# Kernel optimization log

Hardware: AMD Instinct MI355X
Metric: run time of the kernel (lower is better)

The kernel has to match this reference:

```python
import jax, jax.numpy as jnp
import numpy as np

EMBED_DIM = 1024
NUM_HEADS = 16
HEAD_DIM = EMBED_DIM // NUM_HEADS
B, S = 2, 2048


def setup_inputs() -> dict:
    key = jax.random.key(0)
    ks = jax.random.split(key, 9)
    d = EMBED_DIM
    scale = 1.0 / np.sqrt(d)
    inp = {
        "x": jax.random.normal(ks[0], (B, S, d), dtype=jnp.float32),
        "mask": jnp.ones((B, S), dtype=jnp.int32),
        "Wq": jax.random.normal(ks[1], (d, d), dtype=jnp.float32) * scale,
        "bq": jnp.zeros((d,), dtype=jnp.float32),
        "Wk": jax.random.normal(ks[2], (d, d), dtype=jnp.float32) * scale,
        "bk": jnp.zeros((d,), dtype=jnp.float32),
        "Wv": jax.random.normal(ks[3], (d, d), dtype=jnp.float32) * scale,
        "bv": jnp.zeros((d,), dtype=jnp.float32),
        "Wo": jax.random.normal(ks[4], (d, d), dtype=jnp.float32) * scale,
        "bo": jnp.zeros((d,), dtype=jnp.float32),
    }
    return inp


def reference(x, mask, Wq, bq, Wk, bk, Wv, bv, Wo, bo):
    b, s, _ = x.shape
    # projections; torch Linear computes x @ W.T + b
    q = (x @ Wq.T + bq).reshape(b, s, NUM_HEADS, HEAD_DIM).transpose(0, 2, 1, 3)
    k = (x @ Wk.T + bk).reshape(b, s, NUM_HEADS, HEAD_DIM).transpose(0, 2, 1, 3)
    v = (x @ Wv.T + bv).reshape(b, s, NUM_HEADS, HEAD_DIM).transpose(0, 2, 1, 3)
    scores = jnp.einsum("bhqd,bhkd->bhqk", q, k) / np.sqrt(HEAD_DIM)  # (B,H,S,S)
    m = (mask == 0)[:, None, None, :]  # broadcast over heads and query pos
    scores = jnp.where(m, jnp.float32(-1e9), scores)
    attn = jax.nn.softmax(scores, axis=-1)
    out = jnp.einsum("bhqk,bhkd->bhqd", attn, v)
    out = out.transpose(0, 2, 1, 3).reshape(b, s, EMBED_DIM)
    return out @ Wo.T + bo
```

## Files before the change

### kernel.cpp

```cpp
#include <hip/hip_runtime.h>

#define EMBED 1024
#define NHEAD 16
#define HDIM  64
#define BB    2
#define SS    2048

typedef __bf16 bf16x8 __attribute__((ext_vector_type(8)));
typedef float  f32x4  __attribute__((ext_vector_type(4)));
typedef _Float16 f16x4 __attribute__((ext_vector_type(4)));
typedef __fp16 hf16x2 __attribute__((ext_vector_type(2)));

#if defined(__has_builtin)
#if __has_builtin(__builtin_amdgcn_exp2f)
#define EXP2(x) __builtin_amdgcn_exp2f(x)
#else
#define EXP2(x) exp2f(x)
#endif
#else
#define EXP2(x) exp2f(x)
#endif

__device__ __forceinline__ unsigned short f2bf(float f) {
  union { float f; unsigned u; } v; v.f = f;
  unsigned r = v.u + 0x7fffu + ((v.u >> 16) & 1u);
  return (unsigned short)(r >> 16);
}

__device__ __forceinline__ unsigned short f2h(float f) {
  union { _Float16 h; unsigned short u; } t;
  t.h = (_Float16)f;
  return t.u;
}

__device__ __forceinline__ void g2l16(const unsigned short* g, unsigned short* l) {
  __builtin_amdgcn_global_load_lds(
      (const __attribute__((address_space(1))) unsigned int*)g,
      (__attribute__((address_space(3))) unsigned int*)l, 16, 0, 0);
}

__global__ __launch_bounds__(256)
void cvt5_kernel(const float* __restrict__ x,  const float* __restrict__ Wq,
                 const float* __restrict__ Wk, const float* __restrict__ Wv,
                 const float* __restrict__ Wo, const int* __restrict__ mask,
                 unsigned short* __restrict__ xb,  unsigned short* __restrict__ Wqb,
                 unsigned short* __restrict__ Wkb, unsigned short* __restrict__ Wvb,
                 unsigned short* __restrict__ Wob, float* __restrict__ mbias) {
  const int i = blockIdx.x * 256 + threadIdx.x;
  if (i < (1 << 21)) {
    const float* src;
    unsigned short* dst;
    int j;
    if (i < (1 << 20)) {
      src = x; dst = xb; j = i;
    } else {
      const int t = i - (1 << 20);
      const int r = t >> 18;
      j = t & ((1 << 18) - 1);
      src = (r == 0) ? Wq : (r == 1) ? Wk : (r == 2) ? Wv : Wo;
      dst = (r == 0) ? Wqb : (r == 1) ? Wkb : (r == 2) ? Wvb : Wob;
    }
    const float4 f = ((const float4*)src)[j];
    ushort4 u;
    u.x = f2bf(f.x); u.y = f2bf(f.y); u.z = f2bf(f.z); u.w = f2bf(f.w);
    ((ushort4*)dst)[j] = u;
  } else {
    const int j = i - (1 << 21);
    const int4 m = ((const int4*)mask)[j];
    float4 o;
    o.x = m.x ? 0.f : -1e30f; o.y = m.y ? 0.f : -1e30f;
    o.z = m.z ? 0.f : -1e30f; o.w = m.w ? 0.f : -1e30f;
    ((float4*)mbias)[j] = o;
  }
}

template <typename EpiFn>
__device__ __forceinline__
void gemm_core(const unsigned short* __restrict__ A,
               const unsigned short* __restrict__ Bm,
               int m0, int n0, EpiFn epi) {
  __shared__ unsigned short sA[128 * 64];
  __shared__ unsigned short sB[128 * 64];
  const int tid = threadIdx.x;
  const int l  = tid & 63;
  const int w  = tid >> 6;
  const int lm = l & 15;
  const int qd = l >> 4;
  const int wm = w & 1;
  const int wn = w >> 1;

  f32x4 acc[4][4];
#pragma unroll
  for (int i = 0; i < 4; ++i)
#pragma unroll
    for (int j = 0; j < 4; ++j) acc[i][j] = (f32x4){0.f, 0.f, 0.f, 0.f};

  for (int k0 = 0; k0 < EMBED; k0 += 64) {
#pragma unroll
    for (int i = 0; i < 4; ++i) {
      const int t = i * 256 + tid;
      const int r = t >> 3;
      const int c = (t & 7) ^ (r & 7);
      g2l16(A + (m0 + r) * EMBED + k0 + c * 8, &sA[(i * 256 + (w << 6)) * 8]);
      g2l16(Bm + (n0 + r) * EMBED + k0 + c * 8, &sB[(i * 256 + (w << 6)) * 8]);
    }
    __syncthreads();
#pragma unroll
    for (int kk = 0; kk < 2; ++kk) {
      bf16x8 af[4], bfr[4];
#pragma unroll
      for (int mi = 0; mi < 4; ++mi) {
        const int R = wm * 64 + mi * 16 + lm;
        const int ch = R * 8 + (((kk << 2) + qd) ^ (R & 7));
        af[mi] = *(const bf16x8*)&sA[ch * 8];
      }
#pragma unroll
      for (int ni = 0; ni < 4; ++ni) {
        const int R = wn * 64 + ni * 16 + lm;
        const int ch = R * 8 + (((kk << 2) + qd) ^ (R & 7));
        bfr[ni] = *(const bf16x8*)&sB[ch * 8];
      }
#pragma unroll
      for (int mi = 0; mi < 4; ++mi)
#pragma unroll
        for (int ni = 0; ni < 4; ++ni)
          acc[mi][ni] = __builtin_amdgcn_mfma_f32_16x16x32_bf16(
              af[mi], bfr[ni], acc[mi][ni], 0, 0, 0);
    }
    __syncthreads();
  }

#pragma unroll
  for (int mi = 0; mi < 4; ++mi)
#pragma unroll
    for (int ni = 0; ni < 4; ++ni) {
      const int mb = m0 + wm * 64 + mi * 16 + qd * 4;
      const int n  = n0 + wn * 64 + ni * 16 + lm;
      epi(acc[mi][ni], mb, n);
    }
}

__device__ __forceinline__ void decode_tile(int flat, int& a0, int& b0) {
  const int sub = flat & 15;
  const int g = flat >> 4;
  a0 = ((g >> 2) * 2 + (sub >> 3));
  b0 = ((g & 3) * 8 + (sub & 7));
}

__global__ __launch_bounds__(256)
void gemm_qkv(const unsigned short* __restrict__ xb,
              const unsigned short* __restrict__ Wqb,
              const unsigned short* __restrict__ Wkb,
              const unsigned short* __restrict__ Wvb,
              const float* __restrict__ bq, const float* __restrict__ bk,
              const float* __restrict__ bv,
              unsigned short* __restrict__ Qb, unsigned short* __restrict__ Kb,
              unsigned short* __restrict__ VTb) {
  const int z = blockIdx.y;
  int a0, b0;
  decode_tile(blockIdx.x, a0, b0);
  if (z < 2) {
    const unsigned short* A = z ? Wkb : Wqb;
    const float* bias = z ? bk : bq;
    unsigned short* O = z ? Kb : Qb;
    const float scale = z ? 1.0f : 0.125f * 1.4426950408889634f;
    gemm_core(A, xb, a0 * 128, b0 * 128, [&](const f32x4& v, int mb, int n) {
      const float4 bvv = *(const float4*)&bias[mb];
      const int h = mb >> 6, d0 = mb & 63;
      const int b = n >> 11, s = n & 2047;
      ushort4 u;
      u.x = f2bf((v.x + bvv.x) * scale); u.y = f2bf((v.y + bvv.y) * scale);
      u.z = f2bf((v.z + bvv.z) * scale); u.w = f2bf((v.w + bvv.w) * scale);
      *(ushort4*)&O[(((b * NHEAD + h) * SS) + s) * HDIM + d0] = u;
    });
  } else {
    gemm_core(xb, Wvb, b0 * 128, a0 * 128, [&](const f32x4& v, int mb, int n) {
      const float bvv = bv[n];
      const int b = mb >> 11, s = mb & 2047;
      const int h = n >> 6, d = n & 63;
      ushort4 u;
      u.x = f2h(v.x + bvv); u.y = f2h(v.y + bvv);
      u.z = f2h(v.z + bvv); u.w = f2h(v.w + bvv);
      *(ushort4*)&VTb[(((b * NHEAD + h) * HDIM) + d) * SS + s] = u;
    });
  }
}

__global__ __launch_bounds__(256)
void gemm_out(const unsigned short* __restrict__ Wob,
              const unsigned short* __restrict__ Ob,
              const float* __restrict__ bo, float* __restrict__ out) {
  int a0, b0;
  decode_tile(blockIdx.x, a0, b0);
  gemm_core(Wob, Ob, a0 * 128, b0 * 128, [&](const f32x4& v, int mb, int n) {
    const float4 bvv = *(const float4*)&bo[mb];
    float4 o;
    o.x = v.x + bvv.x; o.y = v.y + bvv.y; o.z = v.z + bvv.z; o.w = v.w + bvv.w;
    *(float4*)&out[n * EMBED + mb] = o;
  });
}

__global__ __launch_bounds__(256)
void attn_kernel(const unsigned short* __restrict__ Q,
                 const unsigned short* __restrict__ K,
                 const unsigned short* __restrict__ VT,
                 const float* __restrict__ mbias,
                 unsigned short* __restrict__ Obuf) {
  __shared__ unsigned short sK[64 * 64];
  __shared__ unsigned short sV[64 * 64];
  const int tid = threadIdx.x;
  const int l = tid & 63, w = tid >> 6;
  const int lm = l & 15, qd = l >> 4;
  const int b = blockIdx.z, h = blockIdx.y;
  const int q0 = blockIdx.x * 128 + w * 32;
  const unsigned short* Qh = Q + ((b * NHEAD + h) * SS) * HDIM;
  const unsigned short* Kh = K + ((b * NHEAD + h) * SS) * HDIM;
  const unsigned short* Vh = VT + ((b * NHEAD + h) * HDIM) * SS;
  const float* mb = mbias + b * SS;

  bf16x8 qf[2][2];
#pragma unroll
  for (int g = 0; g < 2; ++g) {
    qf[g][0] = *(const bf16x8*)&Qh[(q0 + g * 16 + lm) * HDIM + qd * 8];
    qf[g][1] = *(const bf16x8*)&Qh[(q0 + g * 16 + lm) * HDIM + 32 + qd * 8];
  }

  f32x4 Od[2][4];
#pragma unroll
  for (int g = 0; g < 2; ++g)
#pragma unroll
    for (int i = 0; i < 4; ++i) Od[g][i] = (f32x4){0.f, 0.f, 0.f, 0.f};
  float lsum[2] = {0.f, 0.f};

  for (int kb = 0; kb < SS; kb += 64) {
#pragma unroll
    for (int i = 0; i < 2; ++i) {
      const int t = i * 256 + tid;
      const int r = t >> 3;
      const int c = (t & 7) ^ (r & 7);
      g2l16(Kh + (kb + r) * HDIM + c * 8, &sK[(i * 256 + (w << 6)) * 8]);
      g2l16(Vh + r * SS + kb + c * 8, &sV[(i * 256 + (w << 6)) * 8]);
    }
    __syncthreads();

    f16x4 pf[2][4];
#pragma unroll
    for (int j = 0; j < 4; ++j) {
      const int R = j * 16 + lm;
      const bf16x8 k0 = *(const bf16x8*)&sK[(R * 8 + (qd ^ (lm & 7))) * 8];
      const bf16x8 k1 = *(const bf16x8*)&sK[(R * 8 + ((4 + qd) ^ (lm & 7))) * 8];
      const float4 bj = *(const float4*)&mb[kb + j * 16 + qd * 4];
      const f32x4 binit = (f32x4){bj.x, bj.y, bj.z, bj.w};
#pragma unroll
      for (int g = 0; g < 2; ++g) {
        f32x4 t0 = binit;
        t0 = __builtin_amdgcn_mfma_f32_16x16x32_bf16(k0, qf[g][0], t0, 0, 0, 0);
        t0 = __builtin_amdgcn_mfma_f32_16x16x32_bf16(k1, qf[g][1], t0, 0, 0, 0);
        const float p0 = EXP2(t0[0]);
        const float p1 = EXP2(t0[1]);
        const float p2 = EXP2(t0[2]);
        const float p3 = EXP2(t0[3]);
        lsum[g] += (p0 + p1) + (p2 + p3);
        union { hf16x2 v[2]; f16x4 f; } pk;
        pk.v[0] = __builtin_amdgcn_cvt_pkrtz(p0, p1);
        pk.v[1] = __builtin_amdgcn_cvt_pkrtz(p2, p3);
        pf[g][j] = pk.f;
      }
    }

#pragma unroll
    for (int dt = 0; dt < 4; ++dt) {
      const int row = dt * 16 + lm;
#pragma unroll
      for (int j = 0; j < 4; ++j) {
        const int ch = (j * 2 + (qd >> 1)) ^ (lm & 7);
        const f16x4 vf = *(const f16x4*)&sV[row * 64 + ch * 8 + (qd & 1) * 4];
#pragma unroll
        for (int g = 0; g < 2; ++g)
          Od[g][dt] = __builtin_amdgcn_mfma_f32_16x16x16f16(vf, pf[g][j],
                                                            Od[g][dt], 0, 0, 0);
      }
    }
    __syncthreads();
  }

#pragma unroll
  for (int g = 0; g < 2; ++g) {
    float ls = lsum[g];
    ls += __shfl_xor(ls, 16);
    ls += __shfl_xor(ls, 32);
    const float rinv = 1.f / ls;
#pragma unroll
    for (int dt = 0; dt < 4; ++dt) {
      ushort4 u;
      u.x = f2bf(Od[g][dt][0] * rinv); u.y = f2bf(Od[g][dt][1] * rinv);
      u.z = f2bf(Od[g][dt][2] * rinv); u.w = f2bf(Od[g][dt][3] * rinv);
      *(ushort4*)&Obuf[(b * SS + q0 + g * 16 + lm) * EMBED + h * HDIM +
                       dt * 16 + qd * 4] = u;
    }
  }
}

extern "C" void kernel_launch(void* const* d_in, const int* in_sizes, int n_in,
                              void* d_out, int out_size, void* d_ws, size_t ws_size,
                              hipStream_t stream) {
  const float* x  = (const float*)d_in[0];
  const int* mask = (const int*)d_in[1];
  const float* Wq = (const float*)d_in[2];
  const float* bq = (const float*)d_in[3];
  const float* Wk = (const float*)d_in[4];
  const float* bk = (const float*)d_in[5];
  const float* Wv = (const float*)d_in[6];
  const float* bv = (const float*)d_in[7];
  const float* Wo = (const float*)d_in[8];
  const float* bo = (const float*)d_in[9];
  float* out = (float*)d_out;

  char* ws = (char*)d_ws;
  unsigned short* xb  = (unsigned short*)(ws);
  unsigned short* Wqb = (unsigned short*)(ws + 8u * 1024 * 1024);
  unsigned short* Wkb = Wqb + 1024 * 1024;
  unsigned short* Wvb = Wkb + 1024 * 1024;
  unsigned short* Wob = Wvb + 1024 * 1024;
  unsigned short* Qb  = (unsigned short*)(ws + 16u * 1024 * 1024);
  unsigned short* Kb  = Qb + 4u * 1024 * 1024;
  unsigned short* VTb = Kb + 4u * 1024 * 1024;
  unsigned short* Ob  = VTb + 4u * 1024 * 1024;
  float* mbb = (float*)(ws + 48u * 1024 * 1024);

  cvt5_kernel<<<8196, 256, 0, stream>>>(x, Wq, Wk, Wv, Wo, mask,
                                        xb, Wqb, Wkb, Wvb, Wob, mbb);
  gemm_qkv<<<dim3(256, 3), 256, 0, stream>>>(xb, Wqb, Wkb, Wvb, bq, bk, bv,
                                             Qb, Kb, VTb);
  attn_kernel<<<dim3(16, 16, 2), 256, 0, stream>>>(Qb, Kb, VTb, mbb, Ob);
  gemm_out<<<256, 256, 0, stream>>>(Wob, Ob, bo, out);
}
```

Baseline: 219.8 us.

## Split attention along the key dimension into two partials and add combine kernel

The attention kernel now splits the key sequence into two halves across an extra grid dimension, doubling the number of blocks. Each half writes an unnormalized bf16 output and its row sums. A new combine kernel adds the two partials and normalizes them before the output projection. The aim is more blocks per CU and better latency hiding on the attention stage. The cost is an extra kernel launch, extra global traffic for the partial buffers, and bf16 rounding of the unnormalized partial outputs.

After: 218.5 us. No clear change (-0.6%).

```diff
diff --git a/kernel.cpp b/kernel.cpp
--- a/kernel.cpp
+++ b/kernel.cpp
@@ -25,6 +25,11 @@
   union { float f; unsigned u; } v; v.f = f;
   unsigned r = v.u + 0x7fffu + ((v.u >> 16) & 1u);
   return (unsigned short)(r >> 16);
+}
+
+__device__ __forceinline__ float bf2f(unsigned short u) {
+  union { unsigned u; float f; } v; v.u = ((unsigned)u) << 16;
+  return v.f;
 }
 
 __device__ __forceinline__ unsigned short f2h(float f) {
@@ -205,18 +210,21 @@
                  const unsigned short* __restrict__ K,
                  const unsigned short* __restrict__ VT,
                  const float* __restrict__ mbias,
-                 unsigned short* __restrict__ Obuf) {
+                 unsigned short* __restrict__ Opart,
+                 float* __restrict__ Lpart) {
   __shared__ unsigned short sK[64 * 64];
   __shared__ unsigned short sV[64 * 64];
   const int tid = threadIdx.x;
   const int l = tid & 63, w = tid >> 6;
   const int lm = l & 15, qd = l >> 4;
-  const int b = blockIdx.z, h = blockIdx.y;
+  const int b = blockIdx.z & 1, sp = blockIdx.z >> 1, h = blockIdx.y;
   const int q0 = blockIdx.x * 128 + w * 32;
   const unsigned short* Qh = Q + ((b * NHEAD + h) * SS) * HDIM;
   const unsigned short* Kh = K + ((b * NHEAD + h) * SS) * HDIM;
   const unsigned short* Vh = VT + ((b * NHEAD + h) * HDIM) * SS;
   const float* mb = mbias + b * SS;
+  unsigned short* Op = Opart + sp * (BB * SS * EMBED);
+  float* Lp = Lpart + sp * (BB * NHEAD * SS);
 
   bf16x8 qf[2][2];
 #pragma unroll
@@ -232,7 +240,8 @@
     for (int i = 0; i < 4; ++i) Od[g][i] = (f32x4){0.f, 0.f, 0.f, 0.f};
   float lsum[2] = {0.f, 0.f};
 
-  for (int kb = 0; kb < SS; kb += 64) {
+  const int kend = sp * (SS / 2) + (SS / 2);
+  for (int kb = sp * (SS / 2); kb < kend; kb += 64) {
 #pragma unroll
     for (int i = 0; i < 2; ++i) {
       const int t = i * 256 + tid;
@@ -289,16 +298,43 @@
     float ls = lsum[g];
     ls += __shfl_xor(ls, 16);
     ls += __shfl_xor(ls, 32);
-    const float rinv = 1.f / ls;
+    if (qd == 0) Lp[(b * NHEAD + h) * SS + q0 + g * 16 + lm] = ls;
 #pragma unroll
     for (int dt = 0; dt < 4; ++dt) {
       ushort4 u;
-      u.x = f2bf(Od[g][dt][0] * rinv); u.y = f2bf(Od[g][dt][1] * rinv);
-      u.z = f2bf(Od[g][dt][2] * rinv); u.w = f2bf(Od[g][dt][3] * rinv);
-      *(ushort4*)&Obuf[(b * SS + q0 + g * 16 + lm) * EMBED + h * HDIM +
-                       dt * 16 + qd * 4] = u;
-    }
-  }
+      u.x = f2bf(Od[g][dt][0]); u.y = f2bf(Od[g][dt][1]);
+      u.z = f2bf(Od[g][dt][2]); u.w = f2bf(Od[g][dt][3]);
+      *(ushort4*)&Op[(b * SS + q0 + g * 16 + lm) * EMBED + h * HDIM +
+                     dt * 16 + qd * 4] = u;
+    }
+  }
+}
+
+__global__ __launch_bounds__(256)
+void combine_kernel(const unsigned short* __restrict__ Opart,
+                    const float* __restrict__ Lpart,
+                    unsigned short* __restrict__ Ob) {
+  const int i = blockIdx.x * 256 + threadIdx.x;
+  const int base = i * 8;
+  const int token = base >> 10;
+  const int h = (base >> 6) & 15;
+  const int b = token >> 11, q = token & 2047;
+  const int lidx = (b * NHEAD + h) * SS + q;
+  const float ls = Lpart[lidx] + Lpart[BB * NHEAD * SS + lidx];
+  const float rinv = 1.f / ls;
+  const ushort4* p0 = (const ushort4*)&Opart[base];
+  const ushort4* p1 = (const ushort4*)&Opart[BB * SS * EMBED + base];
+  ushort4 o[2];
+#pragma unroll
+  for (int k = 0; k < 2; ++k) {
+    const ushort4 a = p0[k], c = p1[k];
+    o[k].x = f2bf((bf2f(a.x) + bf2f(c.x)) * rinv);
+    o[k].y = f2bf((bf2f(a.y) + bf2f(c.y)) * rinv);
+    o[k].z = f2bf((bf2f(a.z) + bf2f(c.z)) * rinv);
+    o[k].w = f2bf((bf2f(a.w) + bf2f(c.w)) * rinv);
+  }
+  *(ushort4*)&Ob[base] = o[0];
+  *(ushort4*)&Ob[base + 4] = o[1];
 }
 
 extern "C" void kernel_launch(void* const* d_in, const int* in_sizes, int n_in,
@@ -317,21 +353,26 @@
   float* out = (float*)d_out;
 
   char* ws = (char*)d_ws;
+  const size_t MB = 1024 * 1024;
   unsigned short* xb  = (unsigned short*)(ws);
-  unsigned short* Wqb = (unsigned short*)(ws + 8u * 1024 * 1024);
+  unsigned short* Ob  = (unsigned short*)(ws);
+  unsigned short* Wqb = (unsigned short*)(ws + 8 * MB);
   unsigned short* Wkb = Wqb + 1024 * 1024;
   unsigned short* Wvb = Wkb + 1024 * 1024;
   unsigned short* Wob = Wvb + 1024 * 1024;
-  unsigned short* Qb  = (unsigned short*)(ws + 16u * 1024 * 1024);
-  unsigned short* Kb  = Qb + 4u * 1024 * 1024;
-  unsigned short* VTb = Kb + 4u * 1024 * 1024;
-  unsigned short* Ob  = VTb + 4u * 1024 * 1024;
-  float* mbb = (float*)(ws + 48u * 1024 * 1024);
+  unsigned short* Qb  = (unsigned short*)(ws + 16 * MB);
+  unsigned short* Kb  = (unsigned short*)(ws + 24 * MB);
+  unsigned short* VTb = (unsigned short*)(ws + 32 * MB);
+  unsigned short* Opart = (unsigned short*)(ws + 40 * MB);
+  float* mbb   = (float*)(ws + 56 * MB);
+  float* Lpart = (float*)(ws + 56 * MB + 64 * 1024);
 
   cvt5_kernel<<<8196, 256, 0, stream>>>(x, Wq, Wk, Wv, Wo, mask,
                                         xb, Wqb, Wkb, Wvb, Wob, mbb);
   gemm_qkv<<<dim3(256, 3), 256, 0, stream>>>(xb, Wqb, Wkb, Wvb, bq, bk, bv,
                                              Qb, Kb, VTb);
-  attn_kernel<<<dim3(16, 16, 2), 256, 0, stream>>>(Qb, Kb, VTb, mbb, Ob);
+  attn_kernel<<<dim3(16, 16, 4), 256, 0, stream>>>(Qb, Kb, VTb, mbb,
+                                                   Opart, Lpart);
+  combine_kernel<<<2048, 256, 0, stream>>>(Opart, Lpart, Ob);
   gemm_out<<<256, 256, 0, stream>>>(Wob, Ob, bo, out);
 }
```
